# Performance work log

Hardware: AMD Instinct MI355X
Metric: run time of the kernel (lower is better)

The kernel has to match this reference:

```python
import jax, jax.numpy as jnp
import numpy as np

NEG_INF = -1e30
EPS = 1e-7  # keras epsilon used by K.ctc_batch_cost


def setup_inputs() -> dict:
    key = jax.random.key(0)
    k1, k2 = jax.random.split(key)
    B, T, C, L = 1024, 256, 128, 32
    logits = jax.random.normal(k1, (B, T, C), dtype=jnp.float32)
    y_pred = jax.nn.softmax(logits, axis=-1)  # ctc_batch_cost expects probabilities
    y_true = jax.random.randint(k2, (B, L), 0, 126, dtype=jnp.int64)
    return {"y_true": y_true, "y_pred": y_pred}


def _ctc_batch_cost(y_true, y_pred):
    # Faithful to K.ctc_batch_cost with input_length=T, label_length=L, blank=C-1
    B, T, C = y_pred.shape
    L = y_true.shape[1]
    blank = C - 1
    S = 2 * L + 1
    logp = jnp.log(y_pred + EPS)  # [B,T,C]

    # extended label sequence: blank, l0, blank, l1, ..., blank  -> [B,S]
    ext = jnp.full((B, S), blank, dtype=jnp.int32)
    ext = ext.at[:, 1::2].set(y_true.astype(jnp.int32))

    # emission log-probs along extended labels: [B,T,S]
    lp_ext = jnp.take_along_axis(logp, ext[:, None, :], axis=2)

    # s-2 skip allowed only for non-blank labels differing from label two back
    is_blank = ext == blank
    same2 = jnp.concatenate(
        [jnp.ones((B, 2), bool), ext[:, 2:] == ext[:, :-2]], axis=1)
    skip_add = jnp.where(is_blank | same2, NEG_INF, 0.0)  # [B,S]

    alpha0 = jnp.full((B, S), NEG_INF, dtype=logp.dtype)
    alpha0 = alpha0.at[:, 0].set(lp_ext[:, 0, 0])
    alpha0 = alpha0.at[:, 1].set(lp_ext[:, 0, 1])

    def shift(x, n):
        return jnp.pad(x, ((0, 0), (n, 0)), constant_values=NEG_INF)[:, :S]

    def step(alpha, lp_t):
        a0 = alpha
        a1 = shift(alpha, 1)
        a2 = jnp.maximum(shift(alpha, 2) + skip_add, NEG_INF)
        m = jnp.maximum(jnp.maximum(a0, a1), a2)
        lse = m + jnp.log(jnp.exp(a0 - m) + jnp.exp(a1 - m) + jnp.exp(a2 - m))
        new = jnp.maximum(lse + lp_t, NEG_INF)
        return new, None

    lp_ext_t = jnp.swapaxes(lp_ext, 0, 1)  # [T,B,S]
    alpha_T, _ = jax.lax.scan(step, alpha0, lp_ext_t[1:])
    final = jnp.logaddexp(alpha_T[:, S - 1], alpha_T[:, S - 2])  # [B]
    return -final[:, None]  # [B,1] like ctc_batch_cost


def reference(y_true, y_pred):
    return _ctc_batch_cost(y_true, y_pred)
```

## Files before the change

### kernel.cpp

```cpp
#include <hip/hip_runtime.h>
#include <hip/hip_bf16.h>


#define CTC_B 1024
#define CTC_T 256
#define CTC_C 128
#define CTC_L 32
#define CTC_BLANK 127
#define CTC_EPS 1e-7f

#define RSTRIDE 33

__global__ __launch_bounds__(256) void ctc_loss_kernel(
    const int* __restrict__ y_true,
    const float* __restrict__ y_pred,
    float* __restrict__ out)
{
    __shared__ float lp[CTC_T * RSTRIDE];

    const int b = blockIdx.x;
    const int tid = threadIdx.x;
    const int lane = tid & 63;
    const int wave = tid >> 6;

    const float* yp = y_pred + (size_t)b * CTC_T * CTC_C;

    int lbl = CTC_BLANK;
    if (lane < CTC_L) lbl = y_true[b * CTC_L + lane];

    {
        const int t0 = wave * 64;
        #pragma unroll 8
        for (int k = 0; k < 64; ++k) {
            int t = t0 + k;
            float p = yp[t * CTC_C + lbl];
            float v = (p + CTC_EPS) * 128.0f;
            if (lane <= 32) lp[t * RSTRIDE + lane] = v;
        }
    }
    __syncthreads();

    if (wave != 0) return;

    double skip = 0.0;
    if (lane >= 1 && lane < CTC_L) {
        int prev = y_true[b * CTC_L + lane - 1];
        if (prev != lbl) skip = 1.0;
    }
    const int lidx = (lane < 32) ? lane : 32;
    const bool alive = (lane < 32);

    double lo = 0.0, hi = 0.0;
    if (lane == 0) {
        lo = (double)lp[32];
        hi = (double)lp[0];
    }

    float lpv_f = lp[RSTRIDE + lidx];
    float lpb_f = lp[RSTRIDE + 32];

    for (int t = 1; t < CTC_T; ++t) {
        float lpv_n = 0.f, lpb_n = 0.f;
        if (t + 1 < CTC_T) {
            lpv_n = lp[(t + 1) * RSTRIDE + lidx];
            lpb_n = lp[(t + 1) * RSTRIDE + 32];
        }
        double pv = alive ? (double)lpv_f : 0.0;
        double pb = (double)lpb_f;

        double ph = __shfl_up(hi, 1);
        if (lane == 0) ph = 0.0;

        double nl = (lo + ph) * pb;
        double nh = (hi + lo + skip * ph) * pv;

        lo = nl; hi = nh;
        lpv_f = lpv_n; lpb_f = lpb_n;
    }

    double aS1 = __shfl(lo, 32);
    double aS2 = __shfl(hi, 31);
    if (lane == 0) {
        out[b] = (float)(1242.1197475634219 - log(aS1 + aS2));
    }
}

extern "C" void kernel_launch(void* const* d_in, const int* in_sizes, int n_in,
                              void* d_out, int out_size, void* d_ws, size_t ws_size,
                              hipStream_t stream) {
    const int*   y_true = (const int*)d_in[0];
    const float* y_pred = (const float*)d_in[1];
    float*       out    = (float*)d_out;

    ctc_loss_kernel<<<CTC_B, 256, 0, stream>>>(y_true, y_pred, out);
}
```

Baseline: 205.1 us.

## Fuse two CTC recurrence time steps per iteration to halve cross-lane shuffles

The alpha recurrence now advances two time steps per loop iteration. Each lane recomputes its left neighbour's intermediate state from two-away shuffles, so the serial shuffle dependency chain is taken once per pair of steps instead of every step. In exchange each iteration does extra double-precision arithmetic and more shared-memory reads, and it adds a peeled first step to keep the step count even.

New measurement: 208.4 us. No clear change (+1.6%).

```diff
diff --git a/kernel.cpp b/kernel.cpp
--- a/kernel.cpp
+++ b/kernel.cpp
@@ -47,7 +47,11 @@
         int prev = y_true[b * CTC_L + lane - 1];
         if (prev != lbl) skip = 1.0;
     }
-    const int lidx = (lane < 32) ? lane : 32;
+    double skipm1 = __shfl_up(skip, 1);
+    if (lane == 0) skipm1 = 0.0;
+
+    const int lidx   = (lane < 32) ? lane : 32;
+    const int lidxm1 = (lidx > 0) ? (lidx - 1) : 0;
     const bool alive = (lane < 32);
 
     double lo = 0.0, hi = 0.0;
@@ -56,26 +60,41 @@
         hi = (double)lp[0];
     }
 
-    float lpv_f = lp[RSTRIDE + lidx];
-    float lpb_f = lp[RSTRIDE + 32];
-
-    for (int t = 1; t < CTC_T; ++t) {
-        float lpv_n = 0.f, lpb_n = 0.f;
-        if (t + 1 < CTC_T) {
-            lpv_n = lp[(t + 1) * RSTRIDE + lidx];
-            lpb_n = lp[(t + 1) * RSTRIDE + 32];
-        }
-        double pv = alive ? (double)lpv_f : 0.0;
-        double pb = (double)lpb_f;
-
+    {
+        float pvf = lp[RSTRIDE + lidx];
+        float pbf = lp[RSTRIDE + 32];
+        double pv = alive ? (double)pvf : 0.0;
+        double pb = (double)pbf;
         double ph = __shfl_up(hi, 1);
         if (lane == 0) ph = 0.0;
-
         double nl = (lo + ph) * pb;
         double nh = (hi + lo + skip * ph) * pv;
+        lo = nl; hi = nh;
+    }
 
-        lo = nl; hi = nh;
-        lpv_f = lpv_n; lpb_f = lpb_n;
+    for (int t = 2; t < CTC_T; t += 2) {
+        double h1 = __shfl_up(hi, 1);
+        double l1 = __shfl_up(lo, 1);
+        double h2 = __shfl_up(hi, 2);
+        if (lane == 0) { h1 = 0.0; l1 = 0.0; }
+        if (lane <= 1) { h2 = 0.0; }
+
+        float pv0f = lp[t * RSTRIDE + lidx];
+        float pm0f = lp[t * RSTRIDE + lidxm1];
+        float pb0f = lp[t * RSTRIDE + 32];
+        float pv1f = lp[(t + 1) * RSTRIDE + lidx];
+        float pb1f = lp[(t + 1) * RSTRIDE + 32];
+        double pv0 = alive ? (double)pv0f : 0.0;
+        double pv1 = alive ? (double)pv1f : 0.0;
+        double pm0 = (double)pm0f;
+        double pb0 = (double)pb0f;
+        double pb1 = (double)pb1f;
+
+        double nl  = (lo + h1) * pb0;
+        double nh  = (hi + lo + skip   * h1) * pv0;
+        double nhm = (h1 + l1 + skipm1 * h2) * pm0;
+        lo = (nl + nhm) * pb1;
+        hi = (nh + nl + skip * nhm) * pv1;
     }
 
     double aS1 = __shfl(lo, 32);
```

## Run CTC forward and backward recursions concurrently, meeting at the midpoint

Applied to the files above, without the earlier changes.

The serial 255-step alpha recursion becomes a forward alpha pass and a backward beta pass that run together in the same wave for about 128 steps each. The loss is recovered as the dot product of alpha and beta at the midpoint, summed with a shuffle reduction. Lane shuffles now use raw ds_bpermute on both halves of each double. The intent is to roughly halve the length of the latency-bound dependency chain, at the cost of more arithmetic and LDS reads per step.

Measured after the change: 203.7 us. About the same (-0.7%).

```diff
diff --git a/kernel.cpp b/kernel.cpp
--- a/kernel.cpp
+++ b/kernel.cpp
@@ -9,7 +9,15 @@
 #define CTC_BLANK 127
 #define CTC_EPS 1e-7f
 
-#define RSTRIDE 33
+#define RSTRIDE 34
+
+__device__ __forceinline__ double bperm_f64(int addr, double v) {
+    union { double d; int i[2]; } u; u.d = v;
+    int x = __builtin_amdgcn_ds_bpermute(addr, u.i[0]);
+    int y = __builtin_amdgcn_ds_bpermute(addr, u.i[1]);
+    union { int i[2]; double d; } r; r.i[0] = x; r.i[1] = y;
+    return r.d;
+}
 
 __global__ __launch_bounds__(256) void ctc_loss_kernel(
     const int* __restrict__ y_true,
@@ -34,8 +42,8 @@
         for (int k = 0; k < 64; ++k) {
             int t = t0 + k;
             float p = yp[t * CTC_C + lbl];
-            float v = (p + CTC_EPS) * 128.0f;
-            if (lane <= 32) lp[t * RSTRIDE + lane] = v;
+            float v = (lane == 33) ? 0.0f : (p + CTC_EPS) * 128.0f;
+            if (lane <= 33) lp[t * RSTRIDE + lane] = v;
         }
     }
     __syncthreads();
@@ -44,44 +52,78 @@
 
     double skip = 0.0;
     if (lane >= 1 && lane < CTC_L) {
-        int prev = y_true[b * CTC_L + lane - 1];
-        if (prev != lbl) skip = 1.0;
+        if (y_true[b * CTC_L + lane - 1] != lbl) skip = 1.0;
     }
+    double skipn = 0.0;
+    if (lane <= 30) {
+        if (y_true[b * CTC_L + lane + 1] != lbl) skipn = 1.0;
+    } else if (lane == 32) {
+        skipn = 1.0;
+    }
+
     const int lidx = (lane < 32) ? lane : 32;
-    const bool alive = (lane < 32);
+    const int pv_idx = (lane < 32) ? lane : 33;
+    const int tn = (lane <= 30) ? (lane + 1)
+                 : (lane == 31) ? 33
+                 : (lane == 32) ? 0
+                 : 32;
+    const int pbi = (lane == 32) ? 33 : 32;
+
+    const int fwd_addr = ((lane + 63) & 63) << 2;
+    const int bwd_addr = (lane == 32) ? 0 : (((lane + 1) & 63) << 2);
 
     double lo = 0.0, hi = 0.0;
     if (lane == 0) {
         lo = (double)lp[32];
         hi = (double)lp[0];
     }
+    double a = 0.0, bb = 0.0;
+    if (lane == 31) { a = 1.0; bb = 1.0; }
 
-    float lpv_f = lp[RSTRIDE + lidx];
-    float lpb_f = lp[RSTRIDE + 32];
+    for (int k = 0; k < 127; ++k) {
+        const int tf = 1 + k;
+        const int tb = 255 - k;
+        float pvf  = lp[tf * RSTRIDE + pv_idx];
+        float pbf  = lp[tf * RSTRIDE + 32];
+        float paf  = lp[tb * RSTRIDE + lidx];
+        float pa1f = lp[tb * RSTRIDE + tn];
+        float pbbf = lp[tb * RSTRIDE + pbi];
 
-    for (int t = 1; t < CTC_T; ++t) {
-        float lpv_n = 0.f, lpb_n = 0.f;
-        if (t + 1 < CTC_T) {
-            lpv_n = lp[(t + 1) * RSTRIDE + lidx];
-            lpb_n = lp[(t + 1) * RSTRIDE + 32];
-        }
-        double pv = alive ? (double)lpv_f : 0.0;
-        double pb = (double)lpb_f;
+        double ph = bperm_f64(fwd_addr, hi);
+        double a1 = bperm_f64(bwd_addr, a);
 
-        double ph = __shfl_up(hi, 1);
-        if (lane == 0) ph = 0.0;
+        double nl = (lo + ph) * (double)pbf;
+        double nh = (hi + lo + skip * ph) * (double)pvf;
+        double v  = (double)pa1f * a1;
+        double u  = (double)pbbf * bb;
+        double nb = u + v;
+        double na = fma((double)paf, a, fma(skipn, v, u));
 
-        double nl = (lo + ph) * pb;
-        double nh = (hi + lo + skip * ph) * pv;
-
-        lo = nl; hi = nh;
-        lpv_f = lpv_n; lpb_f = lpb_n;
+        lo = nl; hi = nh; a = na; bb = nb;
     }
 
-    double aS1 = __shfl(lo, 32);
-    double aS2 = __shfl(hi, 31);
+    {
+        const int tb = 128;
+        float paf  = lp[tb * RSTRIDE + lidx];
+        float pa1f = lp[tb * RSTRIDE + tn];
+        float pbbf = lp[tb * RSTRIDE + pbi];
+        double a1 = bperm_f64(bwd_addr, a);
+        double v  = (double)pa1f * a1;
+        double u  = (double)pbbf * bb;
+        double nb = u + v;
+        double na = fma((double)paf, a, fma(skipn, v, u));
+        a = na; bb = nb;
+    }
+
+    double beA = bperm_f64(32 << 2, a);
+    double beB = bperm_f64(((lane + 63) & 63) << 2, bb);
+    double be = (lane == 0) ? beA : beB;
+    double partial = (lane <= 32) ? (lo * be + hi * a) : 0.0;
+    #pragma unroll
+    for (int off = 32; off >= 1; off >>= 1)
+        partial += __shfl_down(partial, off);
     if (lane == 0) {
-        out[b] = (float)(1242.1197475634219 - log(aS1 + aS2));
+        out[b] = (float)(1242.1197475634219 - log(partial));
     }
 }
 
```
